# Performance work log

Measured on AMD Instinct MI355X. Metric: run time of the kernel, lower is better.

Reference implementation:

```python
import jax, jax.numpy as jnp
import numpy as np

FILTER_SIZE = 4      # pooled output size (wH = wW = 4)
STRIDE = 16          # feature stride -> spatial_scale = 1/16
C = 512              # feature_dim
H = W = 22           # feature map size (352px crop / stride 16)
NI, NS = 3, 64       # images_in_sequence, sequences
KCELLS = 6           # static bound on integer cells overlapped per bin per axis


def setup_inputs() -> dict:
    key = jax.random.key(0)
    k1, k2, k3, k4 = jax.random.split(key, 4)
    feat = jax.random.normal(k1, (NI, NS, C, H, W), dtype=jnp.float32)
    # bb = (x, y, w, h) in image coords; keep boxes inside 352px image
    xy = jax.random.uniform(k2, (NI, NS, 2), minval=0.0, maxval=96.0)
    wh = jax.random.uniform(k3, (NI, NS, 2), minval=64.0, maxval=224.0)
    bb = jnp.concatenate([xy, wh], axis=-1).astype(jnp.float32)
    # conv init: normal(0, sqrt(2/(k*k*out_ch))), zero bias (as in the torch module)
    std = np.float32(np.sqrt(2.0 / (3 * 3 * C)))
    conv_w = jax.random.normal(k4, (C, C, 3, 3), dtype=jnp.float32) * std
    conv_b = jnp.zeros((C,), jnp.float32)
    return {"feat": feat, "bb": bb, "conv_w": conv_w, "conv_b": conv_b}


def _axis_weights(start, end, size):
    """Exact PrRoIPool 1D integration weights on integer grid points.
    start, end: (N, P) continuous bin boundaries in feature coords.
    Returns (N, P, size) weights s.t. integral of the piecewise-linear
    interpolant over [start, end] = sum_i w[i] * f(i)."""
    N, P = start.shape
    s0 = jnp.floor(start).astype(jnp.int32)                  # first cell
    cell = s0[..., None] + jnp.arange(KCELLS, dtype=jnp.int32)  # (N,P,K)
    cf = cell.astype(start.dtype)
    a1 = jnp.maximum(start[..., None], cf)                   # cell-bin intersection
    a2 = jnp.maximum(jnp.minimum(end[..., None], cf + 1.0), a1)
    alpha = a1 - cf
    lim = a2 - cf
    # integral of (1-t) and t over [alpha, lim]  (PrRoIPoolingMatCalculation)
    f0 = (lim - 0.5 * lim * lim) - (alpha - 0.5 * alpha * alpha)  # weight at point `cell`
    f1 = 0.5 * lim * lim - 0.5 * alpha * alpha                    # weight at `cell+1`
    idx0, idx1 = cell, cell + 1
    v0 = (idx0 >= 0) & (idx0 < size)   # out-of-bounds feature reads are 0
    v1 = (idx1 >= 0) & (idx1 < size)
    wts = jnp.concatenate([jnp.where(v0, f0, 0.0), jnp.where(v1, f1, 0.0)], -1)
    idx = jnp.concatenate([jnp.clip(idx0, 0, size - 1), jnp.clip(idx1, 0, size - 1)], -1)
    out = jnp.zeros((N, P, size), start.dtype)
    n_i = jnp.arange(N)[:, None, None]
    p_i = jnp.arange(P)[None, :, None]
    return out.at[n_i, p_i, idx].add(wts)


def prroi_pool(feat, rois, pooled, scale):
    """Precise RoI pooling. feat: (N,C,H,W); rois: (N,4) = (x1,y1,x2,y2),
    image coords; roi i pools from image i. Returns (N,C,pooled,pooled)."""
    x1, y1, x2, y2 = (rois[:, k] * scale for k in range(4))
    bin_w = (x2 - x1) / pooled
    bin_h = (y2 - y1) / pooled
    p = jnp.arange(pooled, dtype=feat.dtype)
    sh = y1[:, None] + p * bin_h[:, None]; eh = sh + bin_h[:, None]   # (N,P)
    sw = x1[:, None] + p * bin_w[:, None]; ew = sw + bin_w[:, None]
    Wy = _axis_weights(sh, eh, feat.shape[2])   # (N,P,H)
    Wx = _axis_weights(sw, ew, feat.shape[3])   # (N,P,W)
    acc = jnp.einsum('nph,nqw,nchw->ncpq', Wy, Wx, feat)
    area = jnp.maximum(bin_h * bin_w, 0.0)[:, None, None, None]
    return jnp.where(area == 0, 0.0, acc / jnp.where(area == 0, 1.0, area))


def reference(feat, bb, conv_w, conv_b):
    ni = feat.shape[0]
    x = feat.reshape(-1, C, H, W)
    x = jax.lax.conv_general_dilated(
        x, conv_w, window_strides=(1, 1), padding=((1, 1), (1, 1)),
        dimension_numbers=('NCHW', 'OIHW', 'NCHW')) + conv_b[None, :, None, None]
    b = bb.reshape(-1, 4)
    rois = jnp.concatenate([b[:, :2], b[:, :2] + b[:, 2:]], axis=-1)  # xyxy
    w = prroi_pool(x, rois, FILTER_SIZE, 1.0 / STRIDE)
    w = w.reshape(ni, -1, C, FILTER_SIZE, FILTER_SIZE).mean(axis=0)   # mean over images
    return w / (C * FILTER_SIZE * FILTER_SIZE)                        # filter_norm
```

## Files before the change

### kernel.cpp

```cpp
#include <hip/hip_runtime.h>


#define NIMG 192
#define CCH 512
#define FH 22
#define FW 22
#define SPATIAL 484
#define KDIM 4608
#define NDIM 1024
#define KQ 8
#define KSEG 576
#define CISTRIDE 1968
#define POOLBLKS 2048

typedef __bf16 bf16;
typedef __bf16 bf16x2 __attribute__((ext_vector_type(2)));
typedef __bf16 bf16x8 __attribute__((ext_vector_type(8)));
typedef float f32x2 __attribute__((ext_vector_type(2)));
typedef float f32x4 __attribute__((ext_vector_type(4)));

#define GLOBAL_AS __attribute__((address_space(1)))
#define LDS_AS __attribute__((address_space(3)))

__device__ __forceinline__ void gload_lds16(const void* g, void* l) {
  __builtin_amdgcn_global_load_lds((GLOBAL_AS const void*)g, (LDS_AS void*)l, 16, 0, 0);
}

__device__ __forceinline__ void axis_range(float a0, float aw, int& r0, int& r1) {
  const float scale = 1.f / 16.f;
  float s1 = a0 * scale;
  float s2 = (a0 + aw) * scale;
  float bl = (s2 - s1) * 0.25f;
  float endv = (s1 + 3 * bl) + bl;
  int c0 = max(0, (int)floorf(s1));
  int c1 = min(21, (int)floorf(endv) + 1);
  r0 = max(0, c0 - 1);
  r1 = min(21, c1 + 1);
}

__device__ __forceinline__ float axis_sum(float a0, float aw, int bin) {
  const float scale = 1.f / 16.f;
  float s1 = a0 * scale;
  float s2 = (a0 + aw) * scale;
  float blen = (s2 - s1) * 0.25f;
  float start = s1 + bin * blen;
  float end = start + blen;
  float inv = 1.0f / blen;
  float S = 0.f;
  int s0i = (int)floorf(start);
  for (int kk = 0; kk < 6; ++kk) {
    int cell = s0i + kk;
    float cf = (float)cell;
    float a1 = fmaxf(start, cf);
    float a2 = fmaxf(fminf(end, cf + 1.f), a1);
    float alpha = a1 - cf, lim = a2 - cf;
    float f0 = (lim - 0.5f * lim * lim) - (alpha - 0.5f * alpha * alpha);
    float f1 = 0.5f * lim * lim - 0.5f * alpha * alpha;
    if (cell >= 0 && cell < 22) S += f0 * inv;
    if (cell + 1 >= 0 && cell + 1 < 22) S += f1 * inv;
  }
  return S;
}

__global__ __launch_bounds__(256, 4) void pool_feat_kernel(
    const float* __restrict__ feat, const float* __restrict__ bb,
    const float* __restrict__ cw, bf16* __restrict__ Wb,
    bf16* __restrict__ Gb) {
  __shared__ __align__(16) char tileb[16 * CISTRIDE];
  __shared__ float wyl[264];
  __shared__ float wxl[264];
  int t = threadIdx.x;
  if (blockIdx.x >= POOLBLKS) {
    int co = blockIdx.x - POOLBLKS;
    float* lw = (float*)tileb;
    const float* src = cw + (long)co * CCH * 9;
    #pragma unroll
    for (int k = 0; k < 18; ++k) lw[t + 256 * k] = src[t + 256 * k];
    __syncthreads();
    bf16* dst = Wb + (long)co * 9 * CCH;
    #pragma unroll
    for (int k = 0; k < 18; ++k) {
      int f = t + 256 * k;
      int pos = f >> 9;
      int ci = f & 511;
      dst[f] = (bf16)lw[ci * 9 + pos];
    }
    return;
  }
  int s = blockIdx.x >> 5;
  int ciq = blockIdx.x & 31;
  int p = t >> 6;
  int lane = t & 63;
  int ci16 = lane & 15;
  int vq = lane >> 4;

  f32x4 A[9];
  #pragma unroll
  for (int a = 0; a < 9; ++a) A[a] = (f32x4){0.f, 0.f, 0.f, 0.f};
  const f32x4* wxp = (const f32x4*)wxl;
  const float* tf = (const float*)tileb;

  for (int img = 0; img < 3; ++img) {
    int n = img * 64 + s;
    int yr0, yr1, xr0, xr1;
    axis_range(bb[n * 4 + 1], bb[n * 4 + 3], yr0, yr1);
    axis_range(bb[n * 4 + 0], bb[n * 4 + 2], xr0, xr1);
    __syncthreads();
    int start16 = (yr0 * 88) & ~15;
    int end16 = ((yr1 + 1) * 88 + 15) & ~15;
    int cpi = (end16 - start16 + 1023) >> 10;
    const float* fpl0 = feat + ((long)n * CCH + ciq * 16) * SPATIAL;
    for (int k = p; k < 16 * cpi; k += 4) {
      int ci = (cpi == 2) ? (k >> 1) : k;
      int c = (cpi == 2) ? (k & 1) : 0;
      int cs = (c == cpi - 1) ? end16 - 1024 : start16;
      if (cs < 0) cs = 0;
      gload_lds16((const char*)(fpl0 + (long)ci * SPATIAL) + cs + lane * 16,
                  tileb + ci * CISTRIDE + cs + lane * 16);
    }
    for (int idx = t; idx < 528; idx += 256)
      (idx < 264 ? wyl[idx] : wxl[idx - 264]) = 0.f;
    __syncthreads();
    if (t < 8) {
      int axis = t >> 2;
      int bin = t & 3;
      const float scale = 1.f / 16.f;
      float a0 = axis ? bb[n * 4 + 0] : bb[n * 4 + 1];
      float aw = axis ? bb[n * 4 + 2] : bb[n * 4 + 3];
      float s1 = a0 * scale;
      float s2 = (a0 + aw) * scale;
      float blen = (s2 - s1) * 0.25f;
      float start = s1 + bin * blen;
      float end = start + blen;
      float inv = 1.0f / blen;
      float* tbl = axis ? wxl : wyl;
      int s0i = (int)floorf(start);
      for (int kk = 0; kk < 6; ++kk) {
        int cell = s0i + kk;
        float cf = (float)cell;
        float a1 = fmaxf(start, cf);
        float a2 = fmaxf(fminf(end, cf + 1.f), a1);
        float alpha = a1 - cf, lim = a2 - cf;
        float f0 = (lim - 0.5f * lim * lim) - (alpha - 0.5f * alpha * alpha);
        float f1 = 0.5f * lim * lim - 0.5f * alpha * alpha;
        if (cell >= 0 && cell < 22) {
          float w = f0 * inv;
          #pragma unroll
          for (int ky = 0; ky < 3; ++ky) {
            int u = cell + ky - 1;
            if (u >= 0 && u < 22) tbl[(ky * 22 + u) * 4 + bin] += w;
          }
        }
        if (cell + 1 >= 0 && cell + 1 < 22) {
          float w = f1 * inv;
          #pragma unroll
          for (int ky = 0; ky < 3; ++ky) {
            int u = cell + ky;
            if (u >= 0 && u < 22) tbl[(ky * 22 + u) * 4 + bin] += w;
          }
        }
      }
    }
    __syncthreads();

    int vbase = xr0 & ~1;
    int npairs = ((xr1 - vbase) >> 1) + 1;
    const f32x2* pl2 = (const f32x2*)(tf + ci16 * (CISTRIDE / 4));

    for (int j = vq; j < npairs; j += 4) {
      int vg = vbase + 2 * j;
      float a00 = 0.f, a01 = 0.f, a10 = 0.f, a11 = 0.f, a20 = 0.f, a21 = 0.f;
      for (int u = yr0; u <= yr1; ++u) {
        f32x2 f = pl2[(u * FW + vg) >> 1];
        float w0 = wyl[u * 4 + p];
        float w1 = wyl[(22 + u) * 4 + p];
        float w2 = wyl[(44 + u) * 4 + p];
        a00 = fmaf(w0, f[0], a00); a01 = fmaf(w0, f[1], a01);
        a10 = fmaf(w1, f[0], a10); a11 = fmaf(w1, f[1], a11);
        a20 = fmaf(w2, f[0], a20); a21 = fmaf(w2, f[1], a21);
      }
      #pragma unroll
      for (int kx = 0; kx < 3; ++kx) {
        f32x4 wx0 = wxp[kx * 22 + vg];
        f32x4 wx1 = wxp[kx * 22 + vg + 1];
        A[kx] += wx0 * a00 + wx1 * a01;
        A[3 + kx] += wx0 * a10 + wx1 * a11;
        A[6 + kx] += wx0 * a20 + wx1 * a21;
      }
    }
  }

  #pragma unroll
  for (int pos = 0; pos < 9; ++pos) {
    #pragma unroll
    for (int q = 0; q < 4; ++q) {
      A[pos][q] += __shfl_xor(A[pos][q], 16);
      A[pos][q] += __shfl_xor(A[pos][q], 32);
    }
  }
  if (vq == 0) {
    int ci = ciq * 16 + ci16;
    #pragma unroll
    for (int pos = 0; pos < 9; ++pos)
      #pragma unroll
      for (int q = 0; q < 4; ++q)
        Gb[(long)(s * 16 + p * 4 + q) * KDIM + pos * CCH + ci] = (bf16)A[pos][q];
  }
}

__global__ __launch_bounds__(256, 2) void gemm_kernel(const bf16* __restrict__ Wb,
                                                      const bf16* __restrict__ Gb,
                                                      float* __restrict__ Opart) {
  __shared__ __align__(16) bf16 As[128 * 64];
  __shared__ __align__(16) bf16 Bs[128 * 64];
  int bid = blockIdx.x;
  int kq = bid & 7;
  int nt = (bid >> 3) & 7;
  int mt = bid >> 6;
  int co0 = mt << 7;
  int n0 = nt << 7;
  int kbase = kq * KSEG;

  int tid = threadIdx.x;
  int wv = tid >> 6, l = tid & 63;
  int wm = wv >> 1, wn = wv & 1;
  int lrow = l >> 3;
  int cg8 = ((l & 7) ^ lrow) << 3;

  long aOff[4], bOff[4];
  #pragma unroll
  for (int j = 0; j < 4; ++j) {
    int row = j * 32 + wv * 8 + lrow;
    aOff[j] = (long)(co0 + row) * KDIM + kbase + cg8;
    bOff[j] = (long)(n0 + row) * KDIM + kbase + cg8;
  }

  const f32x4 vz = {0.f, 0.f, 0.f, 0.f};
  f32x4 acc[4][4];
  #pragma unroll
  for (int a = 0; a < 4; ++a)
    #pragma unroll
    for (int b = 0; b < 4; ++b) acc[a][b] = vz;

  for (int c = 0; c < 9; ++c) {
    long sh = c * 64;
    #pragma unroll
    for (int j = 0; j < 4; ++j) {
      gload_lds16(Wb + aOff[j] + sh, (char*)As + (j * 32 + wv * 8) * 128);
      gload_lds16(Gb + bOff[j] + sh, (char*)Bs + (j * 32 + wv * 8) * 128);
    }
    __syncthreads();
    bf16x8 af[2][4], bfv[2][4];
    #pragma unroll
    for (int kk = 0; kk < 2; ++kk) {
      #pragma unroll
      for (int i = 0; i < 4; ++i) {
        int rowa = wm * 64 + i * 16 + (l & 15);
        int offa = rowa * 128 + kk * 64 + ((l >> 4) * 16);
        offa ^= (rowa & 7) << 4;
        af[kk][i] = *(const bf16x8*)((const char*)As + offa);
        int rowb = wn * 64 + i * 16 + (l & 15);
        int offb = rowb * 128 + kk * 64 + ((l >> 4) * 16);
        offb ^= (rowb & 7) << 4;
        bfv[kk][i] = *(const bf16x8*)((const char*)Bs + offb);
      }
    }
    #pragma unroll
    for (int kk = 0; kk < 2; ++kk)
      #pragma unroll
      for (int mi = 0; mi < 4; ++mi)
        #pragma unroll
        for (int nj = 0; nj < 4; ++nj)
          acc[mi][nj] = __builtin_amdgcn_mfma_f32_16x16x32_bf16(
              af[kk][mi], bfv[kk][nj], acc[mi][nj], 0, 0, 0);
    __syncthreads();
  }

  float* op = Opart + (long)kq * CCH * NDIM;
  #pragma unroll
  for (int nj = 0; nj < 4; ++nj) {
    int nn = n0 + wn * 64 + nj * 16 + (l & 15);
    #pragma unroll
    for (int mi = 0; mi < 4; ++mi) {
      #pragma unroll
      for (int rr = 0; rr < 4; ++rr) {
        int co = co0 + wm * 64 + mi * 16 + (l >> 4) * 4 + rr;
        op[(long)co * NDIM + nn] = acc[mi][nj][rr];
      }
    }
  }
}

__global__ __launch_bounds__(256) void epi_kernel(const float* __restrict__ Opart,
                                                  const float* __restrict__ bb,
                                                  const float* __restrict__ cb,
                                                  float* __restrict__ out) {
  int t4 = blockIdx.x * 256 + threadIdx.x;
  int base = t4 * 4;
  int s = base >> 13;
  int co = (base >> 4) & 511;
  int p = (base >> 2) & 3;
  long osrc = (long)co * NDIM + s * 16 + p * 4;
  f32x4 v = *(const f32x4*)(Opart + osrc);
  #pragma unroll
  for (int kq = 1; kq < KQ; ++kq)
    v += *(const f32x4*)(Opart + (long)kq * CCH * NDIM + osrc);
  f32x4 bf4 = {0.f, 0.f, 0.f, 0.f};
  #pragma unroll
  for (int i = 0; i < 3; ++i) {
    int n = i * 64 + s;
    float Sy = axis_sum(bb[n * 4 + 1], bb[n * 4 + 3], p);
    #pragma unroll
    for (int q = 0; q < 4; ++q)
      bf4[q] += Sy * axis_sum(bb[n * 4 + 0], bb[n * 4 + 2], q);
  }
  const float fin = 1.f / (3.f * 512.f * 16.f);
  v = (v + cb[co] * bf4) * fin;
  *(f32x4*)(out + base) = v;
}

extern "C" void kernel_launch(void* const* d_in, const int* in_sizes, int n_in,
                              void* d_out, int out_size, void* d_ws, size_t ws_size,
                              hipStream_t stream) {
  const float* feat = (const float*)d_in[0];
  const float* bb = (const float*)d_in[1];
  const float* cw = (const float*)d_in[2];
  const float* cb = (const float*)d_in[3];
  float* out = (float*)d_out;

  const size_t WB_BYTES = (size_t)CCH * 9 * CCH * 2;
  const size_t GB_BYTES = (size_t)NDIM * KDIM * 2;
  const size_t OP_BYTES = (size_t)KQ * CCH * NDIM * 4;
  if (ws_size < WB_BYTES + GB_BYTES + OP_BYTES) return;

  char* ws = (char*)d_ws;
  bf16* Wb = (bf16*)ws;
  bf16* Gb = (bf16*)(ws + WB_BYTES);
  float* Opart = (float*)(ws + WB_BYTES + GB_BYTES);

  hipLaunchKernelGGL(pool_feat_kernel, dim3(POOLBLKS + CCH), dim3(256), 0, stream,
                     feat, bb, cw, Wb, Gb);
  hipLaunchKernelGGL(gemm_kernel, dim3(256), dim3(256), 0, stream, Wb, Gb, Opart);
  hipLaunchKernelGGL(epi_kernel, dim3(512), dim3(256), 0, stream, Opart, bb, cb, out);
}
```

Before: 79.85 us.

## Double-buffer feature tiles across images and halve channels per pool block

The pooling kernel now loads each image's feature tile into one of two LDS buffers, so the next image's global-to-LDS copy overlaps the current image's compute, with explicit vmcnt waits. Each block handles 8 channels instead of 16, which doubles the number of pool blocks and lets 8 lane groups split the column pairs. Weight tables for all three images are built once up front instead of per image. In exchange there are more blocks, an extra shuffle-reduction step, and unconditional extra (redundant) loads when cpi is 1.

```diff
diff --git a/kernel.cpp b/kernel.cpp
--- a/kernel.cpp
+++ b/kernel.cpp
@@ -11,7 +11,8 @@
 #define KQ 8
 #define KSEG 576
 #define CISTRIDE 1968
-#define POOLBLKS 2048
+#define TILEB (8 * CISTRIDE)
+#define POOLBLKS 4096
 
 typedef __bf16 bf16;
 typedef __bf16 bf16x2 __attribute__((ext_vector_type(2)));
@@ -66,9 +67,9 @@
     const float* __restrict__ feat, const float* __restrict__ bb,
     const float* __restrict__ cw, bf16* __restrict__ Wb,
     bf16* __restrict__ Gb) {
-  __shared__ __align__(16) char tileb[16 * CISTRIDE];
-  __shared__ float wyl[264];
-  __shared__ float wxl[264];
+  __shared__ __align__(16) char tileb[2 * TILEB];
+  __shared__ float wyl3[3 * 264];
+  __shared__ float wxl3[3 * 264];
   int t = threadIdx.x;
   if (blockIdx.x >= POOLBLKS) {
     int co = blockIdx.x - POOLBLKS;
@@ -87,119 +88,148 @@
     }
     return;
   }
-  int s = blockIdx.x >> 5;
-  int ciq = blockIdx.x & 31;
+  int s = blockIdx.x >> 6;
+  int ciq = blockIdx.x & 63;
   int p = t >> 6;
   int lane = t & 63;
-  int ci16 = lane & 15;
-  int vq = lane >> 4;
+  int ci8 = lane & 7;
+  int vg = lane >> 3;
+
+  int yr0[3], yr1[3], xr0[3], xr1[3], st16[3], en16[3], cpi[3];
+  #pragma unroll
+  for (int i = 0; i < 3; ++i) {
+    int n = i * 64 + s;
+    axis_range(bb[n * 4 + 1], bb[n * 4 + 3], yr0[i], yr1[i]);
+    axis_range(bb[n * 4 + 0], bb[n * 4 + 2], xr0[i], xr1[i]);
+    st16[i] = (yr0[i] * 88) & ~15;
+    en16[i] = ((yr1[i] + 1) * 88 + 15) & ~15;
+    cpi[i] = (en16[i] - st16[i] + 1023) >> 10;
+  }
 
   f32x4 A[9];
   #pragma unroll
   for (int a = 0; a < 9; ++a) A[a] = (f32x4){0.f, 0.f, 0.f, 0.f};
-  const f32x4* wxp = (const f32x4*)wxl;
   const float* tf = (const float*)tileb;
 
-  for (int img = 0; img < 3; ++img) {
+#define STAGE(I, TB)                                                          \
+  {                                                                           \
+    const float* fpl0 =                                                       \
+        feat + ((long)(((I) * 64 + s) * CCH) + ciq * 8) * SPATIAL;            \
+    _Pragma("unroll") for (int kk = 0; kk < 4; ++kk) {                        \
+      int k = p + kk * 4;                                                     \
+      if (k >= 8 * cpi[I]) k = 0;                                             \
+      int ci = (cpi[I] == 2) ? (k >> 1) : k;                                  \
+      int c = (cpi[I] == 2) ? (k & 1) : 0;                                    \
+      int cs = (c == cpi[I] - 1) ? en16[I] - 1024 : st16[I];                  \
+      if (cs < 0) cs = 0;                                                     \
+      gload_lds16((const char*)(fpl0 + (long)ci * SPATIAL) + cs + lane * 16,  \
+                  tileb + (TB) * TILEB + ci * CISTRIDE + cs + lane * 16);     \
+    }                                                                         \
+  }
+
+#define COMPUTE(I, TB)                                                        \
+  {                                                                           \
+    int vbase = xr0[I] & ~1;                                                  \
+    int npairs = ((xr1[I] - vbase) >> 1) + 1;                                 \
+    const float* wy = wyl3 + (I) * 264;                                       \
+    const f32x4* wx = (const f32x4*)(wxl3 + (I) * 264);                       \
+    const f32x2* pl2 =                                                        \
+        (const f32x2*)(tf + (TB) * (TILEB / 4) + ci8 * (CISTRIDE / 4));       \
+    for (int j = vg; j < npairs; j += 8) {                                    \
+      int vgp = vbase + 2 * j;                                                \
+      float a00 = 0.f, a01 = 0.f, a10 = 0.f, a11 = 0.f, a20 = 0.f, a21 = 0.f; \
+      for (int u = yr0[I]; u <= yr1[I]; ++u) {                                \
+        f32x2 f = pl2[(u * FW + vgp) >> 1];                                   \
+        float w0 = wy[u * 4 + p];                                             \
+        float w1 = wy[(22 + u) * 4 + p];                                      \
+        float w2 = wy[(44 + u) * 4 + p];                                      \
+        a00 = fmaf(w0, f[0], a00); a01 = fmaf(w0, f[1], a01);                 \
+        a10 = fmaf(w1, f[0], a10); a11 = fmaf(w1, f[1], a11);                 \
+        a20 = fmaf(w2, f[0], a20); a21 = fmaf(w2, f[1], a21);                 \
+      }                                                                       \
+      _Pragma("unroll") for (int kx = 0; kx < 3; ++kx) {                      \
+        f32x4 wx0 = wx[kx * 22 + vgp];                                        \
+        f32x4 wx1 = wx[kx * 22 + vgp + 1];                                    \
+        A[kx] += wx0 * a00 + wx1 * a01;                                       \
+        A[3 + kx] += wx0 * a10 + wx1 * a11;                                   \
+        A[6 + kx] += wx0 * a20 + wx1 * a21;                                   \
+      }                                                                       \
+    }                                                                         \
+  }
+
+  STAGE(0, 0)
+  STAGE(1, 1)
+  for (int idx = t; idx < 1584; idx += 256)
+    (idx < 792 ? wyl3[idx] : wxl3[idx - 792]) = 0.f;
+  __syncthreads();
+  if (t < 24) {
+    int img = t >> 3;
+    int axis = (t >> 2) & 1;
+    int bin = t & 3;
     int n = img * 64 + s;
-    int yr0, yr1, xr0, xr1;
-    axis_range(bb[n * 4 + 1], bb[n * 4 + 3], yr0, yr1);
-    axis_range(bb[n * 4 + 0], bb[n * 4 + 2], xr0, xr1);
-    __syncthreads();
-    int start16 = (yr0 * 88) & ~15;
-    int end16 = ((yr1 + 1) * 88 + 15) & ~15;
-    int cpi = (end16 - start16 + 1023) >> 10;
-    const float* fpl0 = feat + ((long)n * CCH + ciq * 16) * SPATIAL;
-    for (int k = p; k < 16 * cpi; k += 4) {
-      int ci = (cpi == 2) ? (k >> 1) : k;
-      int c = (cpi == 2) ? (k & 1) : 0;
-      int cs = (c == cpi - 1) ? end16 - 1024 : start16;
-      if (cs < 0) cs = 0;
-      gload_lds16((const char*)(fpl0 + (long)ci * SPATIAL) + cs + lane * 16,
-                  tileb + ci * CISTRIDE + cs + lane * 16);
-    }
-    for (int idx = t; idx < 528; idx += 256)
-      (idx < 264 ? wyl[idx] : wxl[idx - 264]) = 0.f;
-    __syncthreads();
-    if (t < 8) {
-      int axis = t >> 2;
-      int bin = t & 3;
-      const float scale = 1.f / 16.f;
-      float a0 = axis ? bb[n * 4 + 0] : bb[n * 4 + 1];
-      float aw = axis ? bb[n * 4 + 2] : bb[n * 4 + 3];
-      float s1 = a0 * scale;
-      float s2 = (a0 + aw) * scale;
-      float blen = (s2 - s1) * 0.25f;
-      float start = s1 + bin * blen;
-      float end = start + blen;
-      float inv = 1.0f / blen;
-      float* tbl = axis ? wxl : wyl;
-      int s0i = (int)floorf(start);
-      for (int kk = 0; kk < 6; ++kk) {
-        int cell = s0i + kk;
-        float cf = (float)cell;
-        float a1 = fmaxf(start, cf);
-        float a2 = fmaxf(fminf(end, cf + 1.f), a1);
-        float alpha = a1 - cf, lim = a2 - cf;
-        float f0 = (lim - 0.5f * lim * lim) - (alpha - 0.5f * alpha * alpha);
-        float f1 = 0.5f * lim * lim - 0.5f * alpha * alpha;
-        if (cell >= 0 && cell < 22) {
-          float w = f0 * inv;
-          #pragma unroll
-          for (int ky = 0; ky < 3; ++ky) {
-            int u = cell + ky - 1;
-            if (u >= 0 && u < 22) tbl[(ky * 22 + u) * 4 + bin] += w;
-          }
-        }
-        if (cell + 1 >= 0 && cell + 1 < 22) {
-          float w = f1 * inv;
-          #pragma unroll
-          for (int ky = 0; ky < 3; ++ky) {
-            int u = cell + ky;
-            if (u >= 0 && u < 22) tbl[(ky * 22 + u) * 4 + bin] += w;
-          }
+    const float scale = 1.f / 16.f;
+    float a0 = axis ? bb[n * 4 + 0] : bb[n * 4 + 1];
+    float aw = axis ? bb[n * 4 + 2] : bb[n * 4 + 3];
+    float s1 = a0 * scale;
+    float s2 = (a0 + aw) * scale;
+    float blen = (s2 - s1) * 0.25f;
+    float start = s1 + bin * blen;
+    float end = start + blen;
+    float inv = 1.0f / blen;
+    float* tbl = (axis ? wxl3 : wyl3) + img * 264;
+    int s0i = (int)floorf(start);
+    for (int kk = 0; kk < 6; ++kk) {
+      int cell = s0i + kk;
+      float cf = (float)cell;
+      float a1 = fmaxf(start, cf);
+      float a2 = fmaxf(fminf(end, cf + 1.f), a1);
+      float alpha = a1 - cf, lim = a2 - cf;
+      float f0 = (lim - 0.5f * lim * lim) - (alpha - 0.5f * alpha * alpha);
+      float f1 = 0.5f * lim * lim - 0.5f * alpha * alpha;
+      if (cell >= 0 && cell < 22) {
+        float w = f0 * inv;
+        #pragma unroll
+        for (int ky = 0; ky < 3; ++ky) {
+          int u = cell + ky - 1;
+          if (u >= 0 && u < 22) tbl[(ky * 22 + u) * 4 + bin] += w;
         }
       }
-    }
-    __syncthreads();
-
-    int vbase = xr0 & ~1;
-    int npairs = ((xr1 - vbase) >> 1) + 1;
-    const f32x2* pl2 = (const f32x2*)(tf + ci16 * (CISTRIDE / 4));
-
-    for (int j = vq; j < npairs; j += 4) {
-      int vg = vbase + 2 * j;
-      float a00 = 0.f, a01 = 0.f, a10 = 0.f, a11 = 0.f, a20 = 0.f, a21 = 0.f;
-      for (int u = yr0; u <= yr1; ++u) {
-        f32x2 f = pl2[(u * FW + vg) >> 1];
-        float w0 = wyl[u * 4 + p];
-        float w1 = wyl[(22 + u) * 4 + p];
-        float w2 = wyl[(44 + u) * 4 + p];
-        a00 = fmaf(w0, f[0], a00); a01 = fmaf(w0, f[1], a01);
-        a10 = fmaf(w1, f[0], a10); a11 = fmaf(w1, f[1], a11);
-        a20 = fmaf(w2, f[0], a20); a21 = fmaf(w2, f[1], a21);
+      if (cell + 1 >= 0 && cell + 1 < 22) {
+        float w = f1 * inv;
+        #pragma unroll
+        for (int ky = 0; ky < 3; ++ky) {
+          int u = cell + ky;
+          if (u >= 0 && u < 22) tbl[(ky * 22 + u) * 4 + bin] += w;
+        }
       }
-      #pragma unroll
-      for (int kx = 0; kx < 3; ++kx) {
-        f32x4 wx0 = wxp[kx * 22 + vg];
-        f32x4 wx1 = wxp[kx * 22 + vg + 1];
-        A[kx] += wx0 * a00 + wx1 * a01;
-        A[3 + kx] += wx0 * a10 + wx1 * a11;
-        A[6 + kx] += wx0 * a20 + wx1 * a21;
-      }
-    }
-  }
+    }
+  }
+  asm volatile("s_waitcnt vmcnt(4)" ::: "memory");
+  __syncthreads();
+  COMPUTE(0, 0)
+  __syncthreads();
+  STAGE(2, 0)
+  asm volatile("s_waitcnt vmcnt(4)" ::: "memory");
+  __syncthreads();
+  COMPUTE(1, 1)
+  asm volatile("s_waitcnt vmcnt(0)" ::: "memory");
+  __syncthreads();
+  COMPUTE(2, 0)
+
+#undef STAGE
+#undef COMPUTE
 
   #pragma unroll
   for (int pos = 0; pos < 9; ++pos) {
     #pragma unroll
     for (int q = 0; q < 4; ++q) {
+      A[pos][q] += __shfl_xor(A[pos][q], 8);
       A[pos][q] += __shfl_xor(A[pos][q], 16);
       A[pos][q] += __shfl_xor(A[pos][q], 32);
     }
   }
-  if (vq == 0) {
-    int ci = ciq * 16 + ci16;
+  if (vg == 0) {
+    int ci = ciq * 8 + ci8;
     #pragma unroll
     for (int pos = 0; pos < 9; ++pos)
       #pragma unroll
```

Result: slower. 90.85 us (+13.8%).
